# Optimization experiments

Measured on AMD Instinct MI355X. Metric: run time of the kernel, lower is better.

The kernel has to match this reference:

```python
import jax, jax.numpy as jnp
import numpy as np

B, S, DIM, H = 2, 2048, 1024, 16
DH = DIM // H
ROPE_BASE = 10000.0
LOGIT_SCALE_INIT = 2.302585
EPS = 1e-6


def _rotate_half(x):
    # interleaved pairs: out[..., ::2] = -x[..., 1::2]; out[..., 1::2] = x[..., ::2]
    xr = x.reshape(x.shape[:-1] + (x.shape[-1] // 2, 2))
    out = jnp.stack([-xr[..., 1], xr[..., 0]], axis=-1)
    return out.reshape(x.shape)


def _rope_cos_sin(seq_len, head_dim, dtype):
    t = jnp.arange(seq_len, dtype=dtype)
    freqs = 1.0 / ROPE_BASE ** (jnp.arange(0, head_dim, 2, dtype=dtype) / head_dim)
    ang = t[:, None] * freqs[None, :]                # [S, Dh/2]
    emb = jnp.repeat(ang, 2, axis=-1)                # [S, Dh]
    return jnp.cos(emb)[None, None], jnp.sin(emb)[None, None]  # [1,1,S,Dh]


def _l2norm_last(x):
    return x / jnp.sqrt(jnp.sum(x * x, axis=-1, keepdims=True) + EPS)


def setup_inputs() -> dict:
    key = jax.random.key(0)
    ks = jax.random.split(key, 10)
    x = jax.random.normal(ks[0], (B, S, DIM), dtype=jnp.float32)
    # causal mask: True = masked (above diagonal)
    mask = jnp.broadcast_to(jnp.triu(jnp.ones((S, S), dtype=bool), k=1), (B, S, S))
    w = lambda k: jax.random.normal(k, (DIM, DIM), dtype=jnp.float32) * 0.02
    b = lambda k: jax.random.normal(k, (DIM,), dtype=jnp.float32) * 0.01
    return {
        "x": x,
        "Wq": w(ks[1]), "bq": b(ks[2]),
        "Wk": w(ks[3]), "bk": b(ks[4]),
        "Wv": w(ks[5]), "bv": b(ks[6]),
        "Wo": w(ks[7]), "bo": b(ks[8]),
        "logit_scale": jnp.float32(LOGIT_SCALE_INIT),
        "mask": mask,
    }


def reference(x, Wq, bq, Wk, bk, Wv, bv, Wo, bo, logit_scale, mask):
    Bx, Sx, Dm = x.shape
    Dh = Dm // H
    scale = Dh ** -0.5
    # projections (torch Linear: x @ W.T + b), split heads -> [B,H,S,Dh]
    q = (x @ Wq.T + bq).reshape(Bx, Sx, H, Dh).transpose(0, 2, 1, 3)
    k = (x @ Wk.T + bk).reshape(Bx, Sx, H, Dh).transpose(0, 2, 1, 3)
    v = (x @ Wv.T + bv).reshape(Bx, Sx, H, Dh).transpose(0, 2, 1, 3)
    cos, sin = _rope_cos_sin(Sx, Dh, x.dtype)
    q = q * cos + _rotate_half(q) * sin
    k = k * cos + _rotate_half(k) * sin
    q = _l2norm_last(q)
    k = _l2norm_last(k)
    scores = jnp.einsum('bhsd,bhtd->bhst', q, k) * scale * jnp.exp(logit_scale)
    scores = jnp.where(mask[:, None, :, :], -jnp.inf, scores)
    a = jax.nn.softmax(scores, axis=-1)
    out = jnp.einsum('bhst,bhtd->bhsd', a, v).transpose(0, 2, 1, 3).reshape(Bx, Sx, Dm)
    return out @ Wo.T + bo
```

## Files before the change

### kernel.cpp

```cpp
#include <hip/hip_runtime.h>
#include <hip/hip_bf16.h>
#include <math.h>

typedef __hip_bfloat16 bf16;
typedef __attribute__((ext_vector_type(8))) short short8;
typedef __attribute__((ext_vector_type(4))) float floatx4;

static constexpr int Bn = 2, Sn = 2048, Hn = 16, DHn = 64, DIMn = 1024;
static constexpr int Mn = Bn * Sn;

#if __has_builtin(__builtin_amdgcn_exp2f)
#define EXP2(x) __builtin_amdgcn_exp2f(x)
#else
#define EXP2(x) exp2f(x)
#endif

__device__ __forceinline__ unsigned short bfbits(float f) {
  union { __hip_bfloat16 h; unsigned short u; } cv;
  cv.h = __float2bfloat16(f);
  return cv.u;
}

__device__ __forceinline__ float bf2f(unsigned short u) {
  union { float f; unsigned int u; } cv;
  cv.u = ((unsigned int)u) << 16;
  return cv.f;
}

__device__ __forceinline__ unsigned int pack_bf16(float lo, float hi) {
  union { float f; unsigned int u; } a, b;
  a.f = lo; b.f = hi;
  return (b.u & 0xFFFF0000u) | (a.u >> 16);
}

__device__ __forceinline__ void gload_lds16(const void* g, void* l) {
  __builtin_amdgcn_global_load_lds(
      (const __attribute__((address_space(1))) uint32_t*)g,
      (__attribute__((address_space(3))) uint32_t*)l, 16, 0, 0);
}

template <int N>
__device__ __forceinline__ void wait_vm() {
  if constexpr (N == 0) asm volatile("s_waitcnt vmcnt(0)" ::: "memory");
  else if constexpr (N == 2) asm volatile("s_waitcnt vmcnt(2)" ::: "memory");
  else if constexpr (N == 3) asm volatile("s_waitcnt vmcnt(3)" ::: "memory");
  else asm volatile("s_waitcnt vmcnt(4)" ::: "memory");
  __builtin_amdgcn_sched_barrier(0);
}

__global__ void prep_kernel(const float* __restrict__ x,
                            const float* __restrict__ a0, const float* __restrict__ a1,
                            const float* __restrict__ a2, const float* __restrict__ a3,
                            unsigned short* __restrict__ xo,
                            unsigned short* __restrict__ o0, unsigned short* __restrict__ o1,
                            unsigned short* __restrict__ o2, unsigned short* __restrict__ o3,
                            float* __restrict__ tc, float* __restrict__ ts) {
  const int bid = blockIdx.x;
  if (bid < 8192) {
    const float* s;
    unsigned short* d;
    int i;
    if (bid < 4096) {
      s = x; d = xo; i = bid * 256 + threadIdx.x;
    } else {
      int wsel = (bid - 4096) >> 10;
      s = (wsel == 0) ? a0 : (wsel == 1) ? a1 : (wsel == 2) ? a2 : a3;
      d = (wsel == 0) ? o0 : (wsel == 1) ? o1 : (wsel == 2) ? o2 : o3;
      i = ((bid - 4096) & 1023) * 256 + threadIdx.x;
    }
    float4 v = ((const float4*)s)[i];
    ushort4 o;
    o.x = bfbits(v.x); o.y = bfbits(v.y); o.z = bfbits(v.z); o.w = bfbits(v.w);
    ((ushort4*)d)[i] = o;
  } else {
    int t = (bid - 8192) * 256 + threadIdx.x;
    int pos = t >> 5, i = t & 31;
    float f = powf(10000.0f, -(float)i * (1.0f / 32.0f));
    float a = (float)pos * f;
    tc[t] = cosf(a);
    ts[t] = sinf(a);
  }
}

__global__ __launch_bounds__(256, 4) void qkv_kernel(
    const bf16* __restrict__ A,
    const bf16* __restrict__ Wq, const bf16* __restrict__ Wk, const bf16* __restrict__ Wv,
    const float* __restrict__ bq, const float* __restrict__ bk, const float* __restrict__ bv,
    const float* __restrict__ tc, const float* __restrict__ ts,
    unsigned short* __restrict__ qo, unsigned short* __restrict__ ko,
    unsigned short* __restrict__ vt) {
  __shared__ bf16 smem[16384];
  bf16* sAp = smem;
  bf16* sBp = smem + 8192;
  const int sel = blockIdx.y >> 4;
  const bf16* Bw = (sel == 0) ? Wq : (sel == 1) ? Wk : Wv;
  const float* bias = (sel == 0) ? bq : (sel == 1) ? bk : bv;
  const int tid = threadIdx.x;
  const int lane = tid & 63, wave = tid >> 6;
  const int fr = lane & 15, fq = lane >> 4;
  const int m0 = blockIdx.x * 64, n0 = (blockIdx.y & 15) * 64;

  floatx4 acc[4] = {};

  auto stage = [&](int buf, int k0) {
#pragma unroll
    for (int call = 0; call < 2; ++call) {
      int row = call * 32 + (tid >> 3);
      int sb = ((tid & 7) * 16) ^ ((row & 7) << 4);
      gload_lds16(A + (size_t)(m0 + row) * 1024 + k0 + sb / 2,
                  sAp + buf * 4096 + call * 2048 + wave * 512);
    }
#pragma unroll
    for (int call = 0; call < 2; ++call) {
      int row = call * 32 + (tid >> 3);
      int sb = ((tid & 7) * 16) ^ ((row & 7) << 4);
      gload_lds16(Bw + (size_t)(n0 + row) * 1024 + k0 + sb / 2,
                  sBp + buf * 4096 + call * 2048 + wave * 512);
    }
  };

  stage(0, 0);
  stage(1, 64);
  int cur = 0;
  for (int k0 = 0; k0 < 1024; k0 += 64) {
    if (k0 + 64 < 1024) wait_vm<4>(); else wait_vm<0>();
    __builtin_amdgcn_s_barrier();
    __builtin_amdgcn_sched_barrier(0);
    const char* sAc = (const char*)(sAp + cur * 4096);
    const char* sBc = (const char*)(sBp + cur * 4096);
    short8 af[2], bfr[4][2];
    {
      int arow = wave * 16 + fr;
      int asw = (arow & 7) << 4;
#pragma unroll
      for (int kc = 0; kc < 2; ++kc)
        af[kc] = *(const short8*)(sAc + arow * 128 + ((kc * 64 + fq * 16) ^ asw));
    }
#pragma unroll
    for (int ni = 0; ni < 4; ++ni) {
      int brow = ni * 16 + fr;
      int bsw = (brow & 7) << 4;
#pragma unroll
      for (int kc = 0; kc < 2; ++kc)
        bfr[ni][kc] = *(const short8*)(sBc + brow * 128 + ((kc * 64 + fq * 16) ^ bsw));
    }
#pragma unroll
    for (int ni = 0; ni < 4; ++ni)
#pragma unroll
      for (int kc = 0; kc < 2; ++kc)
        acc[ni] = __builtin_amdgcn_mfma_f32_16x16x32_bf16(af[kc], bfr[ni][kc], acc[ni], 0, 0, 0);
    __builtin_amdgcn_sched_barrier(0);
    __builtin_amdgcn_s_barrier();
    if (k0 + 128 < 1024) stage(cur, k0 + 128);
    cur ^= 1;
  }

  if (sel < 2) {
    unsigned short* dst = (sel == 0) ? qo : ko;
    const int h = n0 >> 6;
    float bias_d[4];
#pragma unroll
    for (int ni = 0; ni < 4; ++ni) bias_d[ni] = bias[n0 + ni * 16 + fr];
#pragma unroll
    for (int j = 0; j < 4; ++j) {
      int m = m0 + wave * 16 + fq * 4 + j;
      int b = m >> 11, srow = m & 2047;
      float y[4], ss = 0.f;
#pragma unroll
      for (int ni = 0; ni < 4; ++ni) {
        float val = acc[ni][j] + bias_d[ni];
        float prt = __shfl_xor(val, 1);
        int d = ni * 16 + fr;
        int jj = d >> 1;
        float cc = tc[srow * 32 + jj], sn = ts[srow * 32 + jj];
        y[ni] = (d & 1) ? (val * cc + prt * sn) : (val * cc - prt * sn);
        ss += y[ni] * y[ni];
      }
      ss += __shfl_xor(ss, 1);
      ss += __shfl_xor(ss, 2);
      ss += __shfl_xor(ss, 4);
      ss += __shfl_xor(ss, 8);
      float inv = rsqrtf(ss + 1e-6f);
      size_t ob = ((size_t)(b * 16 + h) * 2048 + srow) * 64;
#pragma unroll
      for (int ni = 0; ni < 4; ++ni)
        dst[ob + ni * 16 + fr] = bfbits(y[ni] * inv);
    }
  } else {
    char* ct = (char*)smem;
#pragma unroll
    for (int ni = 0; ni < 4; ++ni) {
      int nl = ni * 16 + fr;
      float bi = bias[n0 + nl];
#pragma unroll
      for (int j = 0; j < 4; j += 2) {
        int ml = wave * 16 + fq * 4 + j;
        unsigned int u = (unsigned int)bfbits(acc[ni][j] + bi) |
                         ((unsigned int)bfbits(acc[ni][j + 1] + bi) << 16);
        *(unsigned int*)(ct + nl * 128 + ((ml * 2) ^ ((nl & 7) << 4))) = u;
      }
    }
    __syncthreads();
    int nl2 = tid >> 2, ch = tid & 3;
    int h = n0 >> 6;
    int b = m0 >> 11, s0 = m0 & 2047;
    unsigned short* orow = vt + (((size_t)b * 16 + h) * 64 + nl2) * 2048 + s0;
    int swz = (nl2 & 7) << 4;
    int cb = 32 * (ch >> 1) + 16 * (ch & 1);
    union { long long l[2]; short8 v; } s1, s2;
    s1.l[0] = *(const long long*)(ct + nl2 * 128 + ((cb) ^ swz));
    s1.l[1] = *(const long long*)(ct + nl2 * 128 + ((cb + 64) ^ swz));
    s2.l[0] = *(const long long*)(ct + nl2 * 128 + ((cb + 8) ^ swz));
    s2.l[1] = *(const long long*)(ct + nl2 * 128 + ((cb + 72) ^ swz));
    *(short8*)(orow + ch * 16) = s1.v;
    *(short8*)(orow + ch * 16 + 8) = s2.v;
  }
}

__global__ __launch_bounds__(256, 4) void gemm_bt_kernel(
    const bf16* __restrict__ A, const bf16* __restrict__ Bw,
    const float* __restrict__ bias, float* __restrict__ Cf) {
  __shared__ bf16 smem[16384];
  bf16* sAp = smem;
  bf16* sBp = smem + 8192;
  const int tid = threadIdx.x;
  const int lane = tid & 63, wave = tid >> 6;
  const int fr = lane & 15, fq = lane >> 4;
  const int m0 = blockIdx.x * 64, n0 = blockIdx.y * 64;

  floatx4 acc[4] = {};

  auto stage = [&](int buf, int k0) {
#pragma unroll
    for (int call = 0; call < 2; ++call) {
      int row = call * 32 + (tid >> 3);
      int sb = ((tid & 7) * 16) ^ ((row & 7) << 4);
      gload_lds16(A + (size_t)(m0 + row) * 1024 + k0 + sb / 2,
                  sAp + buf * 4096 + call * 2048 + wave * 512);
    }
#pragma unroll
    for (int call = 0; call < 2; ++call) {
      int row = call * 32 + (tid >> 3);
      int sb = ((tid & 7) * 16) ^ ((row & 7) << 4);
      gload_lds16(Bw + (size_t)(n0 + row) * 1024 + k0 + sb / 2,
                  sBp + buf * 4096 + call * 2048 + wave * 512);
    }
  };

  stage(0, 0);
  stage(1, 64);
  int cur = 0;
  for (int k0 = 0; k0 < 1024; k0 += 64) {
    if (k0 + 64 < 1024) wait_vm<4>(); else wait_vm<0>();
    __builtin_amdgcn_s_barrier();
    __builtin_amdgcn_sched_barrier(0);
    const char* sAc = (const char*)(sAp + cur * 4096);
    const char* sBc = (const char*)(sBp + cur * 4096);
    short8 af[2], bfr[4][2];
    {
      int arow = wave * 16 + fr;
      int asw = (arow & 7) << 4;
#pragma unroll
      for (int kc = 0; kc < 2; ++kc)
        af[kc] = *(const short8*)(sAc + arow * 128 + ((kc * 64 + fq * 16) ^ asw));
    }
#pragma unroll
    for (int ni = 0; ni < 4; ++ni) {
      int brow = ni * 16 + fr;
      int bsw = (brow & 7) << 4;
#pragma unroll
      for (int kc = 0; kc < 2; ++kc)
        bfr[ni][kc] = *(const short8*)(sBc + brow * 128 + ((kc * 64 + fq * 16) ^ bsw));
    }
#pragma unroll
    for (int ni = 0; ni < 4; ++ni)
#pragma unroll
      for (int kc = 0; kc < 2; ++kc)
        acc[ni] = __builtin_amdgcn_mfma_f32_16x16x32_bf16(af[kc], bfr[ni][kc], acc[ni], 0, 0, 0);
    __builtin_amdgcn_sched_barrier(0);
    __builtin_amdgcn_s_barrier();
    if (k0 + 128 < 1024) stage(cur, k0 + 128);
    cur ^= 1;
  }

#pragma unroll
  for (int ni = 0; ni < 4; ++ni) {
    int n = n0 + ni * 16 + fr;
    float bi = bias[n];
#pragma unroll
    for (int j = 0; j < 4; ++j) {
      int m = m0 + wave * 16 + fq * 4 + j;
      Cf[(size_t)m * 1024 + n] = acc[ni][j] + bi;
    }
  }
}

__global__ __launch_bounds__(256, 5) void attn_kernel(
    const bf16* __restrict__ qb, const bf16* __restrict__ kb, const bf16* __restrict__ vt,
    const float* __restrict__ ls, unsigned short* __restrict__ out) {
  __shared__ bf16 sK[2][64 * 64];
  __shared__ bf16 sV[2][64 * 64];
  const int bid = blockIdx.x;
  const int rr4 = bid >> 8, g = bid & 255, jj = g & 31;
  const int xq = (rr4 & 1) ? (31 - jj) : jj;
  const int bh = (g >> 5) + 8 * rr4;
  const int q0A = xq * 32, q0B = (63 - xq) * 32;
  const int tid = threadIdx.x;
  const int lane = tid & 63, wave = tid >> 6;
  const int fr = lane & 15, fq = lane >> 4;
  const int myq0 = ((((wave >> 1) ^ bid) & 1)) ? q0B : q0A;
  const int base = myq0 + (wave & 1) * 16;
  float scl2 = __expf(ls[0]) * 0.125f * 1.44269504f;

  const size_t qrow = (size_t)bh * 2048 + base + fr;
  short8 qf0 = *(const short8*)(qb + qrow * 64 + fq * 8);
  short8 qf1 = *(const short8*)(qb + qrow * 64 + 32 + fq * 8);
  asm volatile("" : "+v"(qf0), "+v"(qf1), "+v"(scl2));
  __builtin_amdgcn_sched_barrier(0);

  const bf16* kgb = kb + (size_t)bh * 2048 * 64;
  const bf16* vgb = vt + (size_t)bh * 64 * 2048;

  auto stage = [&](int buf, int t0) {
#pragma unroll
    for (int call = 0; call < 2; ++call) {
      int row = call * 32 + (tid >> 3);
      int sb = ((tid & 7) * 16) ^ ((row & 7) << 4);
      gload_lds16(kgb + (size_t)(t0 + row) * 64 + sb / 2,
                  &sK[buf][call * 2048 + wave * 512]);
    }
#pragma unroll
    for (int call = 0; call < 2; ++call) {
      int row = call * 32 + (tid >> 3);
      int sb = ((tid & 7) * 16) ^ ((row & 7) << 4);
      gload_lds16(vgb + (size_t)row * 2048 + t0 + sb / 2,
                  &sV[buf][call * 2048 + wave * 512]);
    }
  };

  floatx4 oacc[4] = {};
  float m_l = -INFINITY, l_l = 0.f;
  const int qrow_l = base + fr;
  const int rowq = base + fq * 4;
  const int sw = (fr & 7) << 4;

  const int tEnd = q0B + 32;
  stage(0, 0);
  stage(1, 64);
  int cur = 0;
  for (int t0 = 0; t0 < tEnd; t0 += 64) {
    if (t0 + 64 < tEnd) wait_vm<4>(); else wait_vm<0>();
    __builtin_amdgcn_s_barrier();
    __builtin_amdgcn_sched_barrier(0);
    if (t0 < myq0 + 32) {
      const char* sKc = (const char*)sK[cur];
      const char* sVc = (const char*)sV[cur];
      floatx4 sacc[4] = {};
      __builtin_amdgcn_s_setprio(1);
#pragma unroll
      for (int c = 0; c < 4; ++c) {
        int rb = (c * 16 + fr) * 128;
        short8 kf0 = *(const short8*)(sKc + rb + ((fq * 16) ^ sw));
        short8 kf1 = *(const short8*)(sKc + rb + ((64 + fq * 16) ^ sw));
        sacc[c] = __builtin_amdgcn_mfma_f32_16x16x32_bf16(kf0, qf0, sacc[c], 0, 0, 0);
        sacc[c] = __builtin_amdgcn_mfma_f32_16x16x32_bf16(kf1, qf1, sacc[c], 0, 0, 0);
      }
      __builtin_amdgcn_s_setprio(0);
      if (t0 + 63 > base) {
#pragma unroll
        for (int c = 0; c < 4; ++c)
#pragma unroll
          for (int r = 0; r < 4; ++r)
            if ((t0 + c * 16 + fq * 4 + r) > qrow_l) sacc[c][r] = -1e30f;
      }
      float pm0 = fmaxf(fmaxf(sacc[0][0], sacc[0][1]), fmaxf(sacc[0][2], sacc[0][3]));
      float pm1 = fmaxf(fmaxf(sacc[1][0], sacc[1][1]), fmaxf(sacc[1][2], sacc[1][3]));
      float pm2 = fmaxf(fmaxf(sacc[2][0], sacc[2][1]), fmaxf(sacc[2][2], sacc[2][3]));
      float pm3 = fmaxf(fmaxf(sacc[3][0], sacc[3][1]), fmaxf(sacc[3][2], sacc[3][3]));
      float pm = fmaxf(fmaxf(pm0, pm1), fmaxf(pm2, pm3));
      if (!__all(pm * scl2 - m_l <= 11.5f)) {
        float pmr = fmaxf(pm, __shfl_xor(pm, 16));
        pmr = fmaxf(pmr, __shfl_xor(pmr, 32));
        float mnew = fmaxf(m_l, pmr * scl2);
        float rs = EXP2(m_l - mnew);
        m_l = mnew;
        l_l *= rs;
        float rsr[4];
#pragma unroll
        for (int r = 0; r < 4; ++r) rsr[r] = __shfl(rs, rowq - base + r);
#pragma unroll
        for (int d = 0; d < 4; ++d)
#pragma unroll
          for (int r = 0; r < 4; ++r) oacc[d][r] *= rsr[r];
      }
      float p[4][4];
      float ssum = 0.f;
#pragma unroll
      for (int c = 0; c < 4; ++c)
#pragma unroll
        for (int r = 0; r < 4; ++r) {
          p[c][r] = EXP2(sacc[c][r] * scl2 - m_l);
          ssum += p[c][r];
        }
      ssum += __shfl_xor(ssum, 16);
      ssum += __shfl_xor(ssum, 32);
      l_l += ssum;
      short8 pf[2];
#pragma unroll
      for (int kc = 0; kc < 2; ++kc) {
        union { unsigned int w[4]; short8 v; } pk;
        pk.w[0] = pack_bf16(p[kc][0], p[kc][1]);
        pk.w[1] = pack_bf16(p[kc][2], p[kc][3]);
        pk.w[2] = pack_bf16(p[kc + 2][0], p[kc + 2][1]);
        pk.w[3] = pack_bf16(p[kc + 2][2], p[kc + 2][3]);
        pf[kc] = pk.v;
      }
      __builtin_amdgcn_s_setprio(1);
#pragma unroll
      for (int d = 0; d < 4; ++d) {
        int rbv = (d * 16 + fr) * 128;
#pragma unroll
        for (int kc = 0; kc < 2; ++kc) {
          short8 vf = *(const short8*)(sVc + rbv + ((kc * 64 + fq * 16) ^ sw));
          oacc[d] = __builtin_amdgcn_mfma_f32_16x16x32_bf16(pf[kc], vf, oacc[d], 0, 0, 0);
        }
      }
      __builtin_amdgcn_s_setprio(0);
    }
    __builtin_amdgcn_sched_barrier(0);
    __builtin_amdgcn_s_barrier();
    if (t0 + 128 < tEnd) stage(cur, t0 + 128);
    cur ^= 1;
  }
  const int b = bh >> 4, h = bh & 15;
  float il[4];
#pragma unroll
  for (int r = 0; r < 4; ++r) il[r] = 1.0f / __shfl(l_l, rowq - base + r);
#pragma unroll
  for (int r = 0; r < 4; ++r) {
#pragma unroll
    for (int d = 0; d < 4; ++d) {
      size_t o = ((size_t)b * 2048 + rowq + r) * 1024 + h * 64 + d * 16 + fr;
      out[o] = bfbits(oacc[d][r] * il[r]);
    }
  }
}

extern "C" void kernel_launch(void* const* d_in, const int* in_sizes, int n_in,
                              void* d_out, int out_size, void* d_ws, size_t ws_size,
                              hipStream_t stream) {
  (void)in_sizes; (void)n_in; (void)out_size; (void)ws_size;
  const float* x  = (const float*)d_in[0];
  const float* Wq = (const float*)d_in[1];
  const float* bq = (const float*)d_in[2];
  const float* Wk = (const float*)d_in[3];
  const float* bk = (const float*)d_in[4];
  const float* Wv = (const float*)d_in[5];
  const float* bv = (const float*)d_in[6];
  const float* Wo = (const float*)d_in[7];
  const float* bo = (const float*)d_in[8];
  const float* lsc = (const float*)d_in[9];

  uint8_t* w = (uint8_t*)d_ws;
  const size_t MB = 1ull << 20;
  bf16* xb   = (bf16*)(w + 0);
  bf16* wqb  = (bf16*)(w + 8 * MB);
  bf16* wkb  = (bf16*)(w + 10 * MB);
  bf16* wvb  = (bf16*)(w + 12 * MB);
  bf16* wob  = (bf16*)(w + 14 * MB);
  bf16* qbn  = (bf16*)(w + 16 * MB);
  bf16* kbn  = (bf16*)(w + 24 * MB);
  bf16* vtb  = (bf16*)(w + 32 * MB);
  bf16* atb  = (bf16*)(w + 40 * MB);
  float* tc  = (float*)(w + 48 * MB);
  float* ts  = (float*)(w + 48 * MB + 256 * 1024);

  prep_kernel<<<8448, 256, 0, stream>>>(
      x, Wq, Wk, Wv, Wo, (unsigned short*)xb,
      (unsigned short*)wqb, (unsigned short*)wkb, (unsigned short*)wvb,
      (unsigned short*)wob, tc, ts);

  qkv_kernel<<<dim3(64, 48), 256, 0, stream>>>(
      xb, wqb, wkb, wvb, bq, bk, bv, tc, ts,
      (unsigned short*)qbn, (unsigned short*)kbn, (unsigned short*)vtb);

  attn_kernel<<<1024, 256, 0, stream>>>(qbn, kbn, vtb, lsc,
                                        (unsigned short*)atb);

  gemm_bt_kernel<<<dim3(64, 16), 256, 0, stream>>>(atb, wob, bo, (float*)d_out);
}
```

Before: 116.7 us.

## Replace direct global-to-LDS loads with register-staged double-buffered prefetch

The attention loop used to stage K/V tiles with direct global-to-LDS loads and wait on vmcnt before each barrier. It now loads the next tile into registers two iterations ahead, then writes it into the alternate LDS buffer at the start of each iteration, ending with an lgkmcnt wait and a barrier. The aim is to hide global latency behind the MFMA work and to drop the vmcnt stalls. In exchange it uses more VGPRs and issues extra ds_write instructions, and the LDS write at the top of each iteration may stall on the global load that precedes it.

```diff
diff --git a/kernel.cpp b/kernel.cpp
--- a/kernel.cpp
+++ b/kernel.cpp
@@ -321,21 +321,26 @@
   const bf16* kgb = kb + (size_t)bh * 2048 * 64;
   const bf16* vgb = vt + (size_t)bh * 64 * 2048;
 
-  auto stage = [&](int buf, int t0) {
-#pragma unroll
-    for (int call = 0; call < 2; ++call) {
-      int row = call * 32 + (tid >> 3);
-      int sb = ((tid & 7) * 16) ^ ((row & 7) << 4);
-      gload_lds16(kgb + (size_t)(t0 + row) * 64 + sb / 2,
-                  &sK[buf][call * 2048 + wave * 512]);
-    }
-#pragma unroll
-    for (int call = 0; call < 2; ++call) {
-      int row = call * 32 + (tid >> 3);
-      int sb = ((tid & 7) * 16) ^ ((row & 7) << 4);
-      gload_lds16(vgb + (size_t)row * 2048 + t0 + sb / 2,
-                  &sV[buf][call * 2048 + wave * 512]);
-    }
+  const int srow = tid >> 3;
+  const int sb = ((tid & 7) * 16) ^ ((srow & 7) << 4);
+  const bf16* kg0 = kgb + (size_t)srow * 64 + sb / 2;
+  const bf16* kg1 = kgb + (size_t)(32 + srow) * 64 + sb / 2;
+  const bf16* vg0 = vgb + (size_t)srow * 2048 + sb / 2;
+  const bf16* vg1 = vgb + (size_t)(32 + srow) * 2048 + sb / 2;
+  const int wo = wave * 512 + lane * 8;
+
+  short8 rK0, rK1, rV0, rV1;
+  auto stageL = [&](int t0) {
+    rK0 = *(const short8*)(kg0 + (size_t)t0 * 64);
+    rK1 = *(const short8*)(kg1 + (size_t)t0 * 64);
+    rV0 = *(const short8*)(vg0 + t0);
+    rV1 = *(const short8*)(vg1 + t0);
+  };
+  auto stageW = [&](int buf) {
+    *(short8*)(&sK[buf][wo]) = rK0;
+    *(short8*)(&sK[buf][2048 + wo]) = rK1;
+    *(short8*)(&sV[buf][wo]) = rV0;
+    *(short8*)(&sV[buf][2048 + wo]) = rV1;
   };
 
   floatx4 oacc[4] = {};
@@ -345,13 +350,14 @@
   const int sw = (fr & 7) << 4;
 
   const int tEnd = q0B + 32;
-  stage(0, 0);
-  stage(1, 64);
+  stageL(0);
+  stageW(0);
+  stageL(64);
+  __syncthreads();
   int cur = 0;
   for (int t0 = 0; t0 < tEnd; t0 += 64) {
-    if (t0 + 64 < tEnd) wait_vm<4>(); else wait_vm<0>();
-    __builtin_amdgcn_s_barrier();
-    __builtin_amdgcn_sched_barrier(0);
+    if (t0 + 64 < tEnd) stageW(cur ^ 1);
+    if (t0 + 128 < tEnd) stageL(t0 + 128);
     if (t0 < myq0 + 32) {
       const char* sKc = (const char*)sK[cur];
       const char* sVc = (const char*)sV[cur];
@@ -427,9 +433,9 @@
       }
       __builtin_amdgcn_s_setprio(0);
     }
+    asm volatile("s_waitcnt lgkmcnt(0)" ::: "memory");
     __builtin_amdgcn_sched_barrier(0);
     __builtin_amdgcn_s_barrier();
-    if (t0 + 128 < tEnd) stage(cur, t0 + 128);
     cur ^= 1;
   }
   const int b = bh >> 4, h = bh & 15;
@@ -437,13 +443,12 @@
 #pragma unroll
   for (int r = 0; r < 4; ++r) il[r] = 1.0f / __shfl(l_l, rowq - base + r);
 #pragma unroll
-  for (int r = 0; r < 4; ++r) {
+  for (int r = 0; r < 4; ++r)
 #pragma unroll
     for (int d = 0; d < 4; ++d) {
       size_t o = ((size_t)b * 2048 + rowq + r) * 1024 + h * 64 + d * 16 + fr;
       out[o] = bfbits(oacc[d][r] * il[r]);
     }
-  }
 }
 
 extern "C" void kernel_launch(void* const* d_in, const int* in_sizes, int n_in,
```

Result: slower. 128.8 us (+10.4%).

## Enlarge QKV GEMM tile to 128 rows per block for more operand reuse

Applied to the files above, without the earlier changes.

The QKV projection kernel now covers 128 rows of M per block instead of 64. Each wave computes two 16-row fragments against the same B fragments, so each weight tile loaded into LDS is reused across twice as many rows. The A staging buffer, wait counts, grid size and V-transpose epilogue (256-byte rows, wider swizzle) are adjusted to match. The costs are more LDS and registers per block, lower occupancy (launch bounds 3), and half as many blocks (1536) to spread across the CUs.

```diff
diff --git a/kernel.cpp b/kernel.cpp
--- a/kernel.cpp
+++ b/kernel.cpp
@@ -44,7 +44,8 @@
   if constexpr (N == 0) asm volatile("s_waitcnt vmcnt(0)" ::: "memory");
   else if constexpr (N == 2) asm volatile("s_waitcnt vmcnt(2)" ::: "memory");
   else if constexpr (N == 3) asm volatile("s_waitcnt vmcnt(3)" ::: "memory");
-  else asm volatile("s_waitcnt vmcnt(4)" ::: "memory");
+  else if constexpr (N == 4) asm volatile("s_waitcnt vmcnt(4)" ::: "memory");
+  else asm volatile("s_waitcnt vmcnt(6)" ::: "memory");
   __builtin_amdgcn_sched_barrier(0);
 }
 
@@ -82,33 +83,33 @@
   }
 }
 
-__global__ __launch_bounds__(256, 4) void qkv_kernel(
+__global__ __launch_bounds__(256, 3) void qkv_kernel(
     const bf16* __restrict__ A,
     const bf16* __restrict__ Wq, const bf16* __restrict__ Wk, const bf16* __restrict__ Wv,
     const float* __restrict__ bq, const float* __restrict__ bk, const float* __restrict__ bv,
     const float* __restrict__ tc, const float* __restrict__ ts,
     unsigned short* __restrict__ qo, unsigned short* __restrict__ ko,
     unsigned short* __restrict__ vt) {
-  __shared__ bf16 smem[16384];
+  __shared__ bf16 smem[24576];
   bf16* sAp = smem;
-  bf16* sBp = smem + 8192;
+  bf16* sBp = smem + 16384;
   const int sel = blockIdx.y >> 4;
   const bf16* Bw = (sel == 0) ? Wq : (sel == 1) ? Wk : Wv;
   const float* bias = (sel == 0) ? bq : (sel == 1) ? bk : bv;
   const int tid = threadIdx.x;
   const int lane = tid & 63, wave = tid >> 6;
   const int fr = lane & 15, fq = lane >> 4;
-  const int m0 = blockIdx.x * 64, n0 = (blockIdx.y & 15) * 64;
-
-  floatx4 acc[4] = {};
+  const int m0 = blockIdx.x * 128, n0 = (blockIdx.y & 15) * 64;
+
+  floatx4 acc[2][4] = {};
 
   auto stage = [&](int buf, int k0) {
 #pragma unroll
-    for (int call = 0; call < 2; ++call) {
+    for (int call = 0; call < 4; ++call) {
       int row = call * 32 + (tid >> 3);
       int sb = ((tid & 7) * 16) ^ ((row & 7) << 4);
       gload_lds16(A + (size_t)(m0 + row) * 1024 + k0 + sb / 2,
-                  sAp + buf * 4096 + call * 2048 + wave * 512);
+                  sAp + buf * 8192 + call * 2048 + wave * 512);
     }
 #pragma unroll
     for (int call = 0; call < 2; ++call) {
@@ -123,18 +124,19 @@
   stage(1, 64);
   int cur = 0;
   for (int k0 = 0; k0 < 1024; k0 += 64) {
-    if (k0 + 64 < 1024) wait_vm<4>(); else wait_vm<0>();
+    if (k0 + 64 < 1024) wait_vm<6>(); else wait_vm<0>();
     __builtin_amdgcn_s_barrier();
     __builtin_amdgcn_sched_barrier(0);
-    const char* sAc = (const char*)(sAp + cur * 4096);
+    const char* sAc = (const char*)(sAp + cur * 8192);
     const char* sBc = (const char*)(sBp + cur * 4096);
-    short8 af[2], bfr[4][2];
-    {
-      int arow = wave * 16 + fr;
+    short8 af[2][2], bfr[4][2];
+#pragma unroll
+    for (int mi = 0; mi < 2; ++mi) {
+      int arow = wave * 32 + mi * 16 + fr;
       int asw = (arow & 7) << 4;
 #pragma unroll
       for (int kc = 0; kc < 2; ++kc)
-        af[kc] = *(const short8*)(sAc + arow * 128 + ((kc * 64 + fq * 16) ^ asw));
+        af[mi][kc] = *(const short8*)(sAc + arow * 128 + ((kc * 64 + fq * 16) ^ asw));
     }
 #pragma unroll
     for (int ni = 0; ni < 4; ++ni) {
@@ -145,10 +147,13 @@
         bfr[ni][kc] = *(const short8*)(sBc + brow * 128 + ((kc * 64 + fq * 16) ^ bsw));
     }
 #pragma unroll
-    for (int ni = 0; ni < 4; ++ni)
-#pragma unroll
-      for (int kc = 0; kc < 2; ++kc)
-        acc[ni] = __builtin_amdgcn_mfma_f32_16x16x32_bf16(af[kc], bfr[ni][kc], acc[ni], 0, 0, 0);
+    for (int mi = 0; mi < 2; ++mi)
+#pragma unroll
+      for (int ni = 0; ni < 4; ++ni)
+#pragma unroll
+        for (int kc = 0; kc < 2; ++kc)
+          acc[mi][ni] = __builtin_amdgcn_mfma_f32_16x16x32_bf16(af[mi][kc], bfr[ni][kc],
+                                                               acc[mi][ni], 0, 0, 0);
     __builtin_amdgcn_sched_barrier(0);
     __builtin_amdgcn_s_barrier();
     if (k0 + 128 < 1024) stage(cur, k0 + 128);
@@ -162,58 +167,68 @@
 #pragma unroll
     for (int ni = 0; ni < 4; ++ni) bias_d[ni] = bias[n0 + ni * 16 + fr];
 #pragma unroll
-    for (int j = 0; j < 4; ++j) {
-      int m = m0 + wave * 16 + fq * 4 + j;
-      int b = m >> 11, srow = m & 2047;
-      float y[4], ss = 0.f;
+    for (int mi = 0; mi < 2; ++mi)
+#pragma unroll
+      for (int j = 0; j < 4; ++j) {
+        int m = m0 + wave * 32 + mi * 16 + fq * 4 + j;
+        int b = m >> 11, srow = m & 2047;
+        float y[4], ss = 0.f;
+#pragma unroll
+        for (int ni = 0; ni < 4; ++ni) {
+          float val = acc[mi][ni][j] + bias_d[ni];
+          float prt = __shfl_xor(val, 1);
+          int d = ni * 16 + fr;
+          int jj = d >> 1;
+          float cc = tc[srow * 32 + jj], sn = ts[srow * 32 + jj];
+          y[ni] = (d & 1) ? (val * cc + prt * sn) : (val * cc - prt * sn);
+          ss += y[ni] * y[ni];
+        }
+        ss += __shfl_xor(ss, 1);
+        ss += __shfl_xor(ss, 2);
+        ss += __shfl_xor(ss, 4);
+        ss += __shfl_xor(ss, 8);
+        float inv = rsqrtf(ss + 1e-6f);
+        size_t ob = ((size_t)(b * 16 + h) * 2048 + srow) * 64;
+#pragma unroll
+        for (int ni = 0; ni < 4; ++ni)
+          dst[ob + ni * 16 + fr] = bfbits(y[ni] * inv);
+      }
+  } else {
+    __syncthreads();
+    char* ct = (char*)smem;
+#pragma unroll
+    for (int mi = 0; mi < 2; ++mi)
 #pragma unroll
       for (int ni = 0; ni < 4; ++ni) {
-        float val = acc[ni][j] + bias_d[ni];
-        float prt = __shfl_xor(val, 1);
-        int d = ni * 16 + fr;
-        int jj = d >> 1;
-        float cc = tc[srow * 32 + jj], sn = ts[srow * 32 + jj];
-        y[ni] = (d & 1) ? (val * cc + prt * sn) : (val * cc - prt * sn);
-        ss += y[ni] * y[ni];
-      }
-      ss += __shfl_xor(ss, 1);
-      ss += __shfl_xor(ss, 2);
-      ss += __shfl_xor(ss, 4);
-      ss += __shfl_xor(ss, 8);
-      float inv = rsqrtf(ss + 1e-6f);
-      size_t ob = ((size_t)(b * 16 + h) * 2048 + srow) * 64;
-#pragma unroll
-      for (int ni = 0; ni < 4; ++ni)
-        dst[ob + ni * 16 + fr] = bfbits(y[ni] * inv);
-    }
-  } else {
-    char* ct = (char*)smem;
-#pragma unroll
-    for (int ni = 0; ni < 4; ++ni) {
-      int nl = ni * 16 + fr;
-      float bi = bias[n0 + nl];
-#pragma unroll
-      for (int j = 0; j < 4; j += 2) {
-        int ml = wave * 16 + fq * 4 + j;
-        unsigned int u = (unsigned int)bfbits(acc[ni][j] + bi) |
-                         ((unsigned int)bfbits(acc[ni][j + 1] + bi) << 16);
-        *(unsigned int*)(ct + nl * 128 + ((ml * 2) ^ ((nl & 7) << 4))) = u;
-      }
-    }
+        int nl = ni * 16 + fr;
+        float bi = bias[n0 + nl];
+#pragma unroll
+        for (int j = 0; j < 4; j += 2) {
+          int ml = wave * 32 + mi * 16 + fq * 4 + j;
+          unsigned int u = (unsigned int)bfbits(acc[mi][ni][j] + bi) |
+                           ((unsigned int)bfbits(acc[mi][ni][j + 1] + bi) << 16);
+          *(unsigned int*)(ct + nl * 256 + ((ml * 2) ^ ((nl & 15) << 4))) = u;
+        }
+      }
     __syncthreads();
     int nl2 = tid >> 2, ch = tid & 3;
     int h = n0 >> 6;
     int b = m0 >> 11, s0 = m0 & 2047;
     unsigned short* orow = vt + (((size_t)b * 16 + h) * 64 + nl2) * 2048 + s0;
-    int swz = (nl2 & 7) << 4;
+    int swz = (nl2 & 15) << 4;
     int cb = 32 * (ch >> 1) + 16 * (ch & 1);
-    union { long long l[2]; short8 v; } s1, s2;
-    s1.l[0] = *(const long long*)(ct + nl2 * 128 + ((cb) ^ swz));
-    s1.l[1] = *(const long long*)(ct + nl2 * 128 + ((cb + 64) ^ swz));
-    s2.l[0] = *(const long long*)(ct + nl2 * 128 + ((cb + 8) ^ swz));
-    s2.l[1] = *(const long long*)(ct + nl2 * 128 + ((cb + 72) ^ swz));
-    *(short8*)(orow + ch * 16) = s1.v;
-    *(short8*)(orow + ch * 16 + 8) = s2.v;
+    const char* rowp = ct + nl2 * 256;
+#pragma unroll
+    for (int gix = 0; gix < 2; ++gix) {
+      int gb = gix * 128;
+      union { long long l[2]; short8 v; } s1, s2;
+      s1.l[0] = *(const long long*)(rowp + ((gb + cb) ^ swz));
+      s1.l[1] = *(const long long*)(rowp + ((gb + cb + 64) ^ swz));
+      s2.l[0] = *(const long long*)(rowp + ((gb + cb + 8) ^ swz));
+      s2.l[1] = *(const long long*)(rowp + ((gb + cb + 72) ^ swz));
+      *(short8*)(orow + gix * 64 + ch * 16) = s1.v;
+      *(short8*)(orow + gix * 64 + ch * 16 + 8) = s2.v;
+    }
   }
 }
 
@@ -437,13 +452,12 @@
 #pragma unroll
   for (int r = 0; r < 4; ++r) il[r] = 1.0f / __shfl(l_l, rowq - base + r);
 #pragma unroll
-  for (int r = 0; r < 4; ++r) {
+  for (int r = 0; r < 4; ++r)
 #pragma unroll
     for (int d = 0; d < 4; ++d) {
       size_t o = ((size_t)b * 2048 + rowq + r) * 1024 + h * 64 + d * 16 + fr;
       out[o] = bfbits(oacc[d][r] * il[r]);
     }
-  }
 }
 
 extern "C" void kernel_launch(void* const* d_in, const int* in_sizes, int n_in,
@@ -480,7 +494,7 @@
       (unsigned short*)wqb, (unsigned short*)wkb, (unsigned short*)wvb,
       (unsigned short*)wob, tc, ts);
 
-  qkv_kernel<<<dim3(64, 48), 256, 0, stream>>>(
+  qkv_kernel<<<dim3(32, 48), 256, 0, stream>>>(
       xb, wqb, wkb, wvb, bq, bk, bv, tc, ts,
       (unsigned short*)qbn, (unsigned short*)kbn, (unsigned short*)vtb);
 
```

Result: no change. 115.1 us (-1.4%).
